# Kernel tuning notes

Hardware: AMD Instinct MI355X
Metric: run time of the kernel (lower is better)

The kernel has to match this reference:

```python
import jax, jax.numpy as jnp
import numpy as np

B = 512    # batch of signals
N = 1024   # time samples per signal
M = 16384  # frequency grid points (super-resolved)


def setup_inputs() -> dict:
    key = jax.random.key(0)
    x = jax.random.normal(key, (B, 2, N), dtype=jnp.float32)  # [B, 2(re/im), N]
    xgrid = jnp.linspace(-0.5, 0.5, M, dtype=jnp.float32)      # normalized freqs
    return {"x": x, "xgrid": xgrid}


def reference(x, xgrid):
    # x: [B, 2, N] -> complex signal a + i*b
    # Periodogram at arbitrary freqs f: P(f) = |sum_n x_n * exp(-2j*pi*f*n)|^2 / N
    a = x[:, 0]  # real part [B, N]
    b = x[:, 1]  # imag part [B, N]
    Nn = x.shape[-1]
    n = jnp.arange(Nn, dtype=x.dtype)
    phase = (2.0 * jnp.pi) * xgrid[:, None] * n[None, :]  # [M, N]
    C = jnp.cos(phase)  # [M, N]
    S = jnp.sin(phase)  # [M, N]
    # x_n * (cos - i sin) = (a c + b s) + i (b c - a s)
    re = jnp.einsum('bn,mn->bm', a, C) + jnp.einsum('bn,mn->bm', b, S)
    im = jnp.einsum('bn,mn->bm', b, C) - jnp.einsum('bn,mn->bm', a, S)
    return (re * re + im * im) / Nn  # [B, M]
```

## Files before the change

### kernel.cpp

```cpp
#include <hip/hip_runtime.h>


typedef __fp16 half8 __attribute__((ext_vector_type(8)));
typedef __fp16 half2v __attribute__((ext_vector_type(2)));
typedef float f32x4 __attribute__((ext_vector_type(4)));

#define B_SZ 512
#define N_SZ 1024
#define M_SZ 16384
#define BT 128
#define MT 128
#define KT 32

__device__ __forceinline__ unsigned ldsOff(int idx, int k) {
    return (unsigned)(((idx >> 4) << 10) + ((((k >> 3) << 4) + (idx & 15)) << 4) + ((k & 7) << 1));
}

union U2 { half2v h2[2]; uint2 u; };

__global__ __launch_bounds__(256, 2)
void periodogram_kernel(const float* __restrict__ x, const float* __restrict__ xgrid,
                        float* __restrict__ out) {
    __shared__ __align__(16) unsigned char smem[5 * 8192];
    const int tid  = (int)threadIdx.x;
    const int lane = tid & 63;
    const int w    = tid >> 6;
    const int btile = (int)blockIdx.x & 3;
    const int mtile = (int)blockIdx.x >> 2;
    const int b0 = btile * BT;
    const int m0 = mtile * MT;

    const int row8 = tid >> 3;
    const int kk   = (tid & 7) * 4;
    float xg[4];
#pragma unroll
    for (int rep = 0; rep < 4; ++rep) xg[rep] = xgrid[m0 + row8 + rep * 32];

    f32x4 accRe[4][4], accIm[4][4];
#pragma unroll
    for (int i = 0; i < 4; ++i)
#pragma unroll
        for (int j = 0; j < 4; ++j) { accRe[i][j] = (f32x4)0.0f; accIm[i][j] = (f32x4)0.0f; }

    const int wr = (w >> 1) * 64;
    const int wc = (w & 1) * 64;
    const unsigned aBase  = 0u     + (unsigned)((wr >> 4) << 10) + (unsigned)(lane << 4);
    const unsigned bBase  = 8192u  + (unsigned)((wr >> 4) << 10) + (unsigned)(lane << 4);
    const unsigned cBase  = 16384u + (unsigned)((wc >> 4) << 10) + (unsigned)(lane << 4);
    const unsigned sBase  = 24576u + (unsigned)((wc >> 4) << 10) + (unsigned)(lane << 4);
    const unsigned nsBase = 32768u + (unsigned)((wc >> 4) << 10) + (unsigned)(lane << 4);

    for (int t = 0; t < N_SZ / KT; ++t) {
        const int k0 = t * KT;
        __syncthreads();
#pragma unroll
        for (int rep = 0; rep < 4; ++rep) {
            const int row = row8 + rep * 32;
            const unsigned off = ldsOff(row, kk);
            const float4 va = *(const float4*)(x + ((size_t)(b0 + row) * 2 + 0) * N_SZ + k0 + kk);
            const float4 vb = *(const float4*)(x + ((size_t)(b0 + row) * 2 + 1) * N_SZ + k0 + kk);
            U2 pa, pb;
            pa.h2[0] = __builtin_amdgcn_cvt_pkrtz(va.x, va.y);
            pa.h2[1] = __builtin_amdgcn_cvt_pkrtz(va.z, va.w);
            pb.h2[0] = __builtin_amdgcn_cvt_pkrtz(vb.x, vb.y);
            pb.h2[1] = __builtin_amdgcn_cvt_pkrtz(vb.z, vb.w);
            *(uint2*)(smem + 0    + off) = pa.u;
            *(uint2*)(smem + 8192 + off) = pb.u;
            float c[4], s[4];
            const float xgv = xg[rep];
#pragma unroll
            for (int j = 0; j < 4; ++j) {
                const float kf = (float)(k0 + kk + j);
                const float p  = xgv * kf;
                const float e  = __builtin_fmaf(xgv, kf, -p);
                const float f  = (p - floorf(p)) + e;
                c[j] = __builtin_amdgcn_cosf(f);
                s[j] = __builtin_amdgcn_sinf(f);
            }
            U2 pc, ps, pn;
            pc.h2[0] = __builtin_amdgcn_cvt_pkrtz(c[0], c[1]);
            pc.h2[1] = __builtin_amdgcn_cvt_pkrtz(c[2], c[3]);
            ps.h2[0] = __builtin_amdgcn_cvt_pkrtz(s[0], s[1]);
            ps.h2[1] = __builtin_amdgcn_cvt_pkrtz(s[2], s[3]);
            pn.h2[0] = __builtin_amdgcn_cvt_pkrtz(-s[0], -s[1]);
            pn.h2[1] = __builtin_amdgcn_cvt_pkrtz(-s[2], -s[3]);
            *(uint2*)(smem + 16384 + off) = pc.u;
            *(uint2*)(smem + 24576 + off) = ps.u;
            *(uint2*)(smem + 32768 + off) = pn.u;
        }
        __syncthreads();
        half8 fa[4], fb[4];
#pragma unroll
        for (int fm = 0; fm < 4; ++fm) {
            fa[fm] = *(const half8*)(smem + aBase + fm * 1024);
            fb[fm] = *(const half8*)(smem + bBase + fm * 1024);
        }
#pragma unroll
        for (int fn = 0; fn < 4; ++fn) {
            const half8 fc  = *(const half8*)(smem + cBase  + fn * 1024);
            const half8 fs  = *(const half8*)(smem + sBase  + fn * 1024);
            const half8 fns = *(const half8*)(smem + nsBase + fn * 1024);
#pragma unroll
            for (int fm = 0; fm < 4; ++fm) {
                accRe[fm][fn] = __builtin_amdgcn_mfma_f32_16x16x32_f16(fa[fm], fc,  accRe[fm][fn], 0, 0, 0);
                accRe[fm][fn] = __builtin_amdgcn_mfma_f32_16x16x32_f16(fb[fm], fs,  accRe[fm][fn], 0, 0, 0);
                accIm[fm][fn] = __builtin_amdgcn_mfma_f32_16x16x32_f16(fb[fm], fc,  accIm[fm][fn], 0, 0, 0);
                accIm[fm][fn] = __builtin_amdgcn_mfma_f32_16x16x32_f16(fa[fm], fns, accIm[fm][fn], 0, 0, 0);
            }
        }
    }

    const float inv = 1.0f / (float)N_SZ;
    const int orow0 = b0 + wr + ((lane >> 4) << 2);
    const int ocol0 = m0 + wc + (lane & 15);
#pragma unroll
    for (int fm = 0; fm < 4; ++fm)
#pragma unroll
        for (int fn = 0; fn < 4; ++fn) {
            const f32x4 r = accRe[fm][fn];
            const f32x4 im = accIm[fm][fn];
            const int col = ocol0 + fn * 16;
#pragma unroll
            for (int j = 0; j < 4; ++j) {
                const int row = orow0 + fm * 16 + j;
                out[(size_t)row * M_SZ + col] = (r[j] * r[j] + im[j] * im[j]) * inv;
            }
        }
}

extern "C" void kernel_launch(void* const* d_in, const int* in_sizes, int n_in,
                              void* d_out, int out_size, void* d_ws, size_t ws_size,
                              hipStream_t stream) {
    const float* x     = (const float*)d_in[0];
    const float* xgrid = (const float*)d_in[1];
    float* out = (float*)d_out;
    dim3 grid(B_SZ / BT * (M_SZ / MT));
    dim3 block(256);
    periodogram_kernel<<<grid, block, 0, stream>>>(x, xgrid, out);
}
```

Baseline: 77.98 us.

## Generate twiddle fragments in registers via angle recurrence instead of LDS sin/cos tables

Each lane now builds its cos/sin MFMA B-operand fragments directly in registers with a complex-rotation recurrence: step by one sample inside a fragment and by 32 samples between k-steps. This replaces the per-tile sin/cos evaluation and the LDS staging of C, S and -S tables. The signal tiles are staged in LDS in 64-wide k chunks, which halves the number of barriers, and LDS use drops from 40KB to 32KB. The trade-off is accumulated fp32 rounding drift over 1024 recurrence steps, which may degrade accuracy, plus extra VALU work interleaved with the MFMAs.

```diff
diff --git a/kernel.cpp b/kernel.cpp
--- a/kernel.cpp
+++ b/kernel.cpp
@@ -10,31 +10,41 @@
 #define M_SZ 16384
 #define BT 128
 #define MT 128
-#define KT 32
+#define KC 64
+#define KS 32
 
-__device__ __forceinline__ unsigned ldsOff(int idx, int k) {
-    return (unsigned)(((idx >> 4) << 10) + ((((k >> 3) << 4) + (idx & 15)) << 4) + ((k & 7) << 1));
-}
+union H8 { half8 v; half2v h2[4]; };
+union U4 { half2v h2[4]; uint4 u; };
 
-union U2 { half2v h2[2]; uint2 u; };
 
 __global__ __launch_bounds__(256, 2)
 void periodogram_kernel(const float* __restrict__ x, const float* __restrict__ xgrid,
                         float* __restrict__ out) {
-    __shared__ __align__(16) unsigned char smem[5 * 8192];
+    __shared__ __align__(16) unsigned char smem[2 * 16384];
     const int tid  = (int)threadIdx.x;
     const int lane = tid & 63;
     const int w    = tid >> 6;
-    const int btile = (int)blockIdx.x & 3;
-    const int mtile = (int)blockIdx.x >> 2;
-    const int b0 = btile * BT;
-    const int m0 = mtile * MT;
+    const int b0 = ((int)blockIdx.x & 3) * BT;
+    const int m0 = ((int)blockIdx.x >> 2) * MT;
 
-    const int row8 = tid >> 3;
-    const int kk   = (tid & 7) * 4;
-    float xg[4];
+    const int wr = (w >> 1) * 64;
+    const int wc = (w & 1) * 64;
+
+    const float g8f = (float)((lane >> 4) << 3);
+    float cb[4], sb[4], C1[4], S1[4], C32[4], S32[4];
 #pragma unroll
-    for (int rep = 0; rep < 4; ++rep) xg[rep] = xgrid[m0 + row8 + rep * 32];
+    for (int fn = 0; fn < 4; ++fn) {
+        const float xg = xgrid[m0 + wc + fn * 16 + (lane & 15)];
+        float p1 = xg - floorf(xg);
+        C1[fn] = __builtin_amdgcn_cosf(p1);
+        S1[fn] = __builtin_amdgcn_sinf(p1);
+        float p32 = xg * 32.0f; p32 -= floorf(p32);
+        C32[fn] = __builtin_amdgcn_cosf(p32);
+        S32[fn] = __builtin_amdgcn_sinf(p32);
+        float pb = xg * g8f; pb -= floorf(pb);
+        cb[fn] = __builtin_amdgcn_cosf(pb);
+        sb[fn] = __builtin_amdgcn_sinf(pb);
+    }
 
     f32x4 accRe[4][4], accIm[4][4];
 #pragma unroll
@@ -42,70 +52,81 @@
 #pragma unroll
         for (int j = 0; j < 4; ++j) { accRe[i][j] = (f32x4)0.0f; accIm[i][j] = (f32x4)0.0f; }
 
-    const int wr = (w >> 1) * 64;
-    const int wc = (w & 1) * 64;
-    const unsigned aBase  = 0u     + (unsigned)((wr >> 4) << 10) + (unsigned)(lane << 4);
-    const unsigned bBase  = 8192u  + (unsigned)((wr >> 4) << 10) + (unsigned)(lane << 4);
-    const unsigned cBase  = 16384u + (unsigned)((wc >> 4) << 10) + (unsigned)(lane << 4);
-    const unsigned sBase  = 24576u + (unsigned)((wc >> 4) << 10) + (unsigned)(lane << 4);
-    const unsigned nsBase = 32768u + (unsigned)((wc >> 4) << 10) + (unsigned)(lane << 4);
+    const int srow = tid >> 1;
+    const int skh  = tid & 1;
+    const float* srcA = x + (size_t)(b0 + srow) * 2048 + (size_t)(skh * 32);
+    const float* srcB = srcA + 1024;
+    const unsigned wbase = (unsigned)(((srow >> 4) * 2 + skh) * 1024 + ((srow & 15) << 4));
 
-    for (int t = 0; t < N_SZ / KT; ++t) {
-        const int k0 = t * KT;
+    const unsigned rbaseW = (unsigned)((wr >> 4) * 2048 + (lane << 4));
+
+    for (int ch = 0; ch < N_SZ / KC; ++ch) {
+        const int k0c = ch * KC;
+        __syncthreads();
+        {
+            const float4* pa = (const float4*)(srcA + k0c);
+            const float4* pb = (const float4*)(srcB + k0c);
+#pragma unroll
+            for (int g = 0; g < 4; ++g) {
+                const float4 v0 = pa[2 * g], v1 = pa[2 * g + 1];
+                U4 u;
+                u.h2[0] = __builtin_amdgcn_cvt_pkrtz(v0.x, v0.y);
+                u.h2[1] = __builtin_amdgcn_cvt_pkrtz(v0.z, v0.w);
+                u.h2[2] = __builtin_amdgcn_cvt_pkrtz(v1.x, v1.y);
+                u.h2[3] = __builtin_amdgcn_cvt_pkrtz(v1.z, v1.w);
+                *(uint4*)(smem + wbase + g * 256) = u.u;
+            }
+#pragma unroll
+            for (int g = 0; g < 4; ++g) {
+                const float4 v0 = pb[2 * g], v1 = pb[2 * g + 1];
+                U4 u;
+                u.h2[0] = __builtin_amdgcn_cvt_pkrtz(v0.x, v0.y);
+                u.h2[1] = __builtin_amdgcn_cvt_pkrtz(v0.z, v0.w);
+                u.h2[2] = __builtin_amdgcn_cvt_pkrtz(v1.x, v1.y);
+                u.h2[3] = __builtin_amdgcn_cvt_pkrtz(v1.z, v1.w);
+                *(uint4*)(smem + 16384 + wbase + g * 256) = u.u;
+            }
+        }
         __syncthreads();
 #pragma unroll
-        for (int rep = 0; rep < 4; ++rep) {
-            const int row = row8 + rep * 32;
-            const unsigned off = ldsOff(row, kk);
-            const float4 va = *(const float4*)(x + ((size_t)(b0 + row) * 2 + 0) * N_SZ + k0 + kk);
-            const float4 vb = *(const float4*)(x + ((size_t)(b0 + row) * 2 + 1) * N_SZ + k0 + kk);
-            U2 pa, pb;
-            pa.h2[0] = __builtin_amdgcn_cvt_pkrtz(va.x, va.y);
-            pa.h2[1] = __builtin_amdgcn_cvt_pkrtz(va.z, va.w);
-            pb.h2[0] = __builtin_amdgcn_cvt_pkrtz(vb.x, vb.y);
-            pb.h2[1] = __builtin_amdgcn_cvt_pkrtz(vb.z, vb.w);
-            *(uint2*)(smem + 0    + off) = pa.u;
-            *(uint2*)(smem + 8192 + off) = pb.u;
-            float c[4], s[4];
-            const float xgv = xg[rep];
-#pragma unroll
-            for (int j = 0; j < 4; ++j) {
-                const float kf = (float)(k0 + kk + j);
-                const float p  = xgv * kf;
-                const float e  = __builtin_fmaf(xgv, kf, -p);
-                const float f  = (p - floorf(p)) + e;
-                c[j] = __builtin_amdgcn_cosf(f);
-                s[j] = __builtin_amdgcn_sinf(f);
-            }
-            U2 pc, ps, pn;
-            pc.h2[0] = __builtin_amdgcn_cvt_pkrtz(c[0], c[1]);
-            pc.h2[1] = __builtin_amdgcn_cvt_pkrtz(c[2], c[3]);
-            ps.h2[0] = __builtin_amdgcn_cvt_pkrtz(s[0], s[1]);
-            ps.h2[1] = __builtin_amdgcn_cvt_pkrtz(s[2], s[3]);
-            pn.h2[0] = __builtin_amdgcn_cvt_pkrtz(-s[0], -s[1]);
-            pn.h2[1] = __builtin_amdgcn_cvt_pkrtz(-s[2], -s[3]);
-            *(uint2*)(smem + 16384 + off) = pc.u;
-            *(uint2*)(smem + 24576 + off) = ps.u;
-            *(uint2*)(smem + 32768 + off) = pn.u;
-        }
-        __syncthreads();
-        half8 fa[4], fb[4];
-#pragma unroll
-        for (int fm = 0; fm < 4; ++fm) {
-            fa[fm] = *(const half8*)(smem + aBase + fm * 1024);
-            fb[fm] = *(const half8*)(smem + bBase + fm * 1024);
-        }
-#pragma unroll
-        for (int fn = 0; fn < 4; ++fn) {
-            const half8 fc  = *(const half8*)(smem + cBase  + fn * 1024);
-            const half8 fs  = *(const half8*)(smem + sBase  + fn * 1024);
-            const half8 fns = *(const half8*)(smem + nsBase + fn * 1024);
+        for (int s = 0; s < 2; ++s) {
+            const unsigned ab = rbaseW + (unsigned)(s * 1024);
+            half8 fa[4], fb[4];
 #pragma unroll
             for (int fm = 0; fm < 4; ++fm) {
-                accRe[fm][fn] = __builtin_amdgcn_mfma_f32_16x16x32_f16(fa[fm], fc,  accRe[fm][fn], 0, 0, 0);
-                accRe[fm][fn] = __builtin_amdgcn_mfma_f32_16x16x32_f16(fb[fm], fs,  accRe[fm][fn], 0, 0, 0);
-                accIm[fm][fn] = __builtin_amdgcn_mfma_f32_16x16x32_f16(fb[fm], fc,  accIm[fm][fn], 0, 0, 0);
-                accIm[fm][fn] = __builtin_amdgcn_mfma_f32_16x16x32_f16(fa[fm], fns, accIm[fm][fn], 0, 0, 0);
+                fa[fm] = *(const half8*)(smem + ab + fm * 2048);
+                fb[fm] = *(const half8*)(smem + 16384 + ab + fm * 2048);
+            }
+#pragma unroll
+            for (int fn = 0; fn < 4; ++fn) {
+                H8 fc, fs, fns;
+                float cj = cb[fn], sj = sb[fn];
+#pragma unroll
+                for (int jp = 0; jp < 4; ++jp) {
+                    const float t1 = sj * S1[fn];
+                    const float co = __builtin_fmaf(cj, C1[fn], -t1);
+                    const float t2 = cj * S1[fn];
+                    const float so = __builtin_fmaf(sj, C1[fn], t2);
+                    fc.h2[jp]  = __builtin_amdgcn_cvt_pkrtz(cj, co);
+                    fs.h2[jp]  = __builtin_amdgcn_cvt_pkrtz(sj, so);
+                    fns.h2[jp] = __builtin_amdgcn_cvt_pkrtz(-sj, -so);
+                    const float t3 = so * S1[fn];
+                    cj = __builtin_fmaf(co, C1[fn], -t3);
+                    const float t4 = co * S1[fn];
+                    sj = __builtin_fmaf(so, C1[fn], t4);
+                }
+#pragma unroll
+                for (int fm = 0; fm < 4; ++fm) {
+                    accRe[fm][fn] = __builtin_amdgcn_mfma_f32_16x16x32_f16(fa[fm], fc.v,  accRe[fm][fn], 0, 0, 0);
+                    accRe[fm][fn] = __builtin_amdgcn_mfma_f32_16x16x32_f16(fb[fm], fs.v,  accRe[fm][fn], 0, 0, 0);
+                    accIm[fm][fn] = __builtin_amdgcn_mfma_f32_16x16x32_f16(fb[fm], fc.v,  accIm[fm][fn], 0, 0, 0);
+                    accIm[fm][fn] = __builtin_amdgcn_mfma_f32_16x16x32_f16(fa[fm], fns.v, accIm[fm][fn], 0, 0, 0);
+                }
+                const float r1 = sb[fn] * S32[fn];
+                const float ncb = __builtin_fmaf(cb[fn], C32[fn], -r1);
+                const float r2 = cb[fn] * S32[fn];
+                const float nsb = __builtin_fmaf(sb[fn], C32[fn], r2);
+                cb[fn] = ncb; sb[fn] = nsb;
             }
         }
     }
```

Result: slower. 126.3 us (+61.9%).

## Replace per-element sin/cos with rotation recurrence, swizzle LDS, prefetch loads

Applied to the files above, without the earlier changes.

Per-tile sin/cos evaluation is replaced by an angle-addition recurrence. Each thread computes base rotations once and then advances four consecutive samples and the next-tile start with FMAs. The negated-sine LDS buffer is dropped in favour of a sign-bit XOR on fragments. An XOR swizzle is added to the LDS layout to reduce bank conflicts, and global loads plus twiddle computation are moved ahead of the first barrier so they overlap the previous tile's MFMAs. The recurrence accumulates rounding error over the 32 tile steps, which may affect accuracy.

```diff
diff --git a/kernel.cpp b/kernel.cpp
--- a/kernel.cpp
+++ b/kernel.cpp
@@ -12,29 +12,48 @@
 #define MT 128
 #define KT 32
 
-__device__ __forceinline__ unsigned ldsOff(int idx, int k) {
-    return (unsigned)(((idx >> 4) << 10) + ((((k >> 3) << 4) + (idx & 15)) << 4) + ((k & 7) << 1));
-}
+union U2  { half2v h2[2]; uint2 u; };
+union H8U { half8 v; uint4 u; };
 
-union U2 { half2v h2[2]; uint2 u; };
 
 __global__ __launch_bounds__(256, 2)
 void periodogram_kernel(const float* __restrict__ x, const float* __restrict__ xgrid,
                         float* __restrict__ out) {
-    __shared__ __align__(16) unsigned char smem[5 * 8192];
+    __shared__ __align__(16) unsigned char smem[4 * 8192];
     const int tid  = (int)threadIdx.x;
     const int lane = tid & 63;
     const int w    = tid >> 6;
-    const int btile = (int)blockIdx.x & 3;
-    const int mtile = (int)blockIdx.x >> 2;
-    const int b0 = btile * BT;
-    const int m0 = mtile * MT;
+    const int b0 = ((int)blockIdx.x & 3) * BT;
+    const int m0 = ((int)blockIdx.x >> 2) * MT;
 
     const int row8 = tid >> 3;
     const int kk   = (tid & 7) * 4;
-    float xg[4];
+    const int g    = kk >> 3;
+    const int kkh  = (kk >> 2) & 1;
+
+    unsigned woff[4];
+    const float* srcA[4];
+    float C1[4], S1[4], C32[4], S32[4], c0v[4], s0v[4];
 #pragma unroll
-    for (int rep = 0; rep < 4; ++rep) xg[rep] = xgrid[m0 + row8 + rep * 32];
+    for (int rep = 0; rep < 4; ++rep) {
+        const int row = row8 + rep * 32;
+        const int rb = row >> 4, r16 = row & 15;
+        woff[rep] = (unsigned)(rb * 1024 + ((g * 16 + (r16 ^ (g << 1))) << 4) + kkh * 8);
+        srcA[rep] = x + (size_t)(b0 + row) * 2048 + kk;
+        const float xg = xgrid[m0 + row];
+        const float f1 = xg - floorf(xg);
+        C1[rep] = __builtin_amdgcn_cosf(f1);
+        S1[rep] = __builtin_amdgcn_sinf(f1);
+        float p32 = xg * 32.0f; p32 -= floorf(p32);
+        C32[rep] = __builtin_amdgcn_cosf(p32);
+        S32[rep] = __builtin_amdgcn_sinf(p32);
+        const float kf = (float)kk;
+        const float pk = xg * kf;
+        const float e  = __builtin_fmaf(xg, kf, -pk);
+        const float f  = (pk - floorf(pk)) + e;
+        c0v[rep] = __builtin_amdgcn_cosf(f);
+        s0v[rep] = __builtin_amdgcn_sinf(f);
+    }
 
     f32x4 accRe[4][4], accIm[4][4];
 #pragma unroll
@@ -44,49 +63,51 @@
 
     const int wr = (w >> 1) * 64;
     const int wc = (w & 1) * 64;
-    const unsigned aBase  = 0u     + (unsigned)((wr >> 4) << 10) + (unsigned)(lane << 4);
-    const unsigned bBase  = 8192u  + (unsigned)((wr >> 4) << 10) + (unsigned)(lane << 4);
-    const unsigned cBase  = 16384u + (unsigned)((wc >> 4) << 10) + (unsigned)(lane << 4);
-    const unsigned sBase  = 24576u + (unsigned)((wc >> 4) << 10) + (unsigned)(lane << 4);
-    const unsigned nsBase = 32768u + (unsigned)((wc >> 4) << 10) + (unsigned)(lane << 4);
+    const unsigned roff  = (unsigned)((lane ^ ((lane >> 4) << 1)) << 4);
+    const unsigned aBase = 0u     + ((unsigned)(wr >> 4) << 10) + roff;
+    const unsigned bBase = 8192u  + ((unsigned)(wr >> 4) << 10) + roff;
+    const unsigned cBase = 16384u + ((unsigned)(wc >> 4) << 10) + roff;
+    const unsigned sBase = 24576u + ((unsigned)(wc >> 4) << 10) + roff;
 
     for (int t = 0; t < N_SZ / KT; ++t) {
         const int k0 = t * KT;
+        float4 va[4], vb[4];
+#pragma unroll
+        for (int rep = 0; rep < 4; ++rep) {
+            va[rep] = *(const float4*)(srcA[rep] + k0);
+            vb[rep] = *(const float4*)(srcA[rep] + k0 + 1024);
+        }
+        uint2 cw[4], sw[4];
+#pragma unroll
+        for (int rep = 0; rep < 4; ++rep) {
+            const float c0 = c0v[rep], s0 = s0v[rep];
+            const float c1 = __builtin_fmaf(c0, C1[rep], -(s0 * S1[rep]));
+            const float s1 = __builtin_fmaf(s0, C1[rep],  (c0 * S1[rep]));
+            const float c2 = __builtin_fmaf(c1, C1[rep], -(s1 * S1[rep]));
+            const float s2 = __builtin_fmaf(s1, C1[rep],  (c1 * S1[rep]));
+            const float c3 = __builtin_fmaf(c2, C1[rep], -(s2 * S1[rep]));
+            const float s3 = __builtin_fmaf(s2, C1[rep],  (c2 * S1[rep]));
+            U2 pc, ps;
+            pc.h2[0] = __builtin_amdgcn_cvt_pkrtz(c0, c1);
+            pc.h2[1] = __builtin_amdgcn_cvt_pkrtz(c2, c3);
+            ps.h2[0] = __builtin_amdgcn_cvt_pkrtz(s0, s1);
+            ps.h2[1] = __builtin_amdgcn_cvt_pkrtz(s2, s3);
+            cw[rep] = pc.u; sw[rep] = ps.u;
+            c0v[rep] = __builtin_fmaf(c0, C32[rep], -(s0 * S32[rep]));
+            s0v[rep] = __builtin_fmaf(s0, C32[rep],  (c0 * S32[rep]));
+        }
         __syncthreads();
 #pragma unroll
         for (int rep = 0; rep < 4; ++rep) {
-            const int row = row8 + rep * 32;
-            const unsigned off = ldsOff(row, kk);
-            const float4 va = *(const float4*)(x + ((size_t)(b0 + row) * 2 + 0) * N_SZ + k0 + kk);
-            const float4 vb = *(const float4*)(x + ((size_t)(b0 + row) * 2 + 1) * N_SZ + k0 + kk);
             U2 pa, pb;
-            pa.h2[0] = __builtin_amdgcn_cvt_pkrtz(va.x, va.y);
-            pa.h2[1] = __builtin_amdgcn_cvt_pkrtz(va.z, va.w);
-            pb.h2[0] = __builtin_amdgcn_cvt_pkrtz(vb.x, vb.y);
-            pb.h2[1] = __builtin_amdgcn_cvt_pkrtz(vb.z, vb.w);
-            *(uint2*)(smem + 0    + off) = pa.u;
-            *(uint2*)(smem + 8192 + off) = pb.u;
-            float c[4], s[4];
-            const float xgv = xg[rep];
-#pragma unroll
-            for (int j = 0; j < 4; ++j) {
-                const float kf = (float)(k0 + kk + j);
-                const float p  = xgv * kf;
-                const float e  = __builtin_fmaf(xgv, kf, -p);
-                const float f  = (p - floorf(p)) + e;
-                c[j] = __builtin_amdgcn_cosf(f);
-                s[j] = __builtin_amdgcn_sinf(f);
-            }
-            U2 pc, ps, pn;
-            pc.h2[0] = __builtin_amdgcn_cvt_pkrtz(c[0], c[1]);
-            pc.h2[1] = __builtin_amdgcn_cvt_pkrtz(c[2], c[3]);
-            ps.h2[0] = __builtin_amdgcn_cvt_pkrtz(s[0], s[1]);
-            ps.h2[1] = __builtin_amdgcn_cvt_pkrtz(s[2], s[3]);
-            pn.h2[0] = __builtin_amdgcn_cvt_pkrtz(-s[0], -s[1]);
-            pn.h2[1] = __builtin_amdgcn_cvt_pkrtz(-s[2], -s[3]);
-            *(uint2*)(smem + 16384 + off) = pc.u;
-            *(uint2*)(smem + 24576 + off) = ps.u;
-            *(uint2*)(smem + 32768 + off) = pn.u;
+            pa.h2[0] = __builtin_amdgcn_cvt_pkrtz(va[rep].x, va[rep].y);
+            pa.h2[1] = __builtin_amdgcn_cvt_pkrtz(va[rep].z, va[rep].w);
+            pb.h2[0] = __builtin_amdgcn_cvt_pkrtz(vb[rep].x, vb[rep].y);
+            pb.h2[1] = __builtin_amdgcn_cvt_pkrtz(vb[rep].z, vb[rep].w);
+            *(uint2*)(smem + 0     + woff[rep]) = pa.u;
+            *(uint2*)(smem + 8192  + woff[rep]) = pb.u;
+            *(uint2*)(smem + 16384 + woff[rep]) = cw[rep];
+            *(uint2*)(smem + 24576 + woff[rep]) = sw[rep];
         }
         __syncthreads();
         half8 fa[4], fb[4];
@@ -97,15 +118,19 @@
         }
 #pragma unroll
         for (int fn = 0; fn < 4; ++fn) {
-            const half8 fc  = *(const half8*)(smem + cBase  + fn * 1024);
-            const half8 fs  = *(const half8*)(smem + sBase  + fn * 1024);
-            const half8 fns = *(const half8*)(smem + nsBase + fn * 1024);
+            const half8 fc = *(const half8*)(smem + cBase + fn * 1024);
+            H8U fsU;  fsU.v = *(const half8*)(smem + sBase + fn * 1024);
+            H8U fnsU;
+            fnsU.u.x = fsU.u.x ^ 0x80008000u;
+            fnsU.u.y = fsU.u.y ^ 0x80008000u;
+            fnsU.u.z = fsU.u.z ^ 0x80008000u;
+            fnsU.u.w = fsU.u.w ^ 0x80008000u;
 #pragma unroll
             for (int fm = 0; fm < 4; ++fm) {
-                accRe[fm][fn] = __builtin_amdgcn_mfma_f32_16x16x32_f16(fa[fm], fc,  accRe[fm][fn], 0, 0, 0);
-                accRe[fm][fn] = __builtin_amdgcn_mfma_f32_16x16x32_f16(fb[fm], fs,  accRe[fm][fn], 0, 0, 0);
-                accIm[fm][fn] = __builtin_amdgcn_mfma_f32_16x16x32_f16(fb[fm], fc,  accIm[fm][fn], 0, 0, 0);
-                accIm[fm][fn] = __builtin_amdgcn_mfma_f32_16x16x32_f16(fa[fm], fns, accIm[fm][fn], 0, 0, 0);
+                accRe[fm][fn] = __builtin_amdgcn_mfma_f32_16x16x32_f16(fa[fm], fc,     accRe[fm][fn], 0, 0, 0);
+                accRe[fm][fn] = __builtin_amdgcn_mfma_f32_16x16x32_f16(fb[fm], fsU.v,  accRe[fm][fn], 0, 0, 0);
+                accIm[fm][fn] = __builtin_amdgcn_mfma_f32_16x16x32_f16(fb[fm], fc,     accIm[fm][fn], 0, 0, 0);
+                accIm[fm][fn] = __builtin_amdgcn_mfma_f32_16x16x32_f16(fa[fm], fnsU.v, accIm[fm][fn], 0, 0, 0);
             }
         }
     }
```

After: 67.24 us. 1.16x faster.
